# Kernel tuning notes

Measured on AMD Instinct MI355X. Metric: run time of the kernel, lower is better.

## Reference

```python
import jax, jax.numpy as jnp
import numpy as np
from jax import lax

I = 2048   # input_size
H = 2048   # hidden_size
T = 512    # window_size
L = 4      # num_layers


def setup_inputs() -> dict:
    key = jax.random.key(0)
    ks = jax.random.split(key, 8)
    s = 1.0 / np.sqrt(H)  # PyTorch RNN init scale
    x = jax.random.normal(ks[0], (I, T), dtype=jnp.float32)
    # input_size == hidden_size, so all layers' W_ih share shape (H, H)
    w_ih = jax.random.uniform(ks[1], (L, H, H), minval=-s, maxval=s, dtype=jnp.float32)
    w_hh = jax.random.uniform(ks[2], (L, H, H), minval=-s, maxval=s, dtype=jnp.float32)
    b_ih = jax.random.uniform(ks[3], (L, H), minval=-s, maxval=s, dtype=jnp.float32)
    b_hh = jax.random.uniform(ks[4], (L, H), minval=-s, maxval=s, dtype=jnp.float32)
    w_fc = jax.random.uniform(ks[5], (I, H), minval=-s, maxval=s, dtype=jnp.float32)
    b_fc = jax.random.uniform(ks[6], (I,), minval=-s, maxval=s, dtype=jnp.float32)
    return {"x": x, "w_ih": w_ih, "w_hh": w_hh, "b_ih": b_ih, "b_hh": b_hh,
            "w_fc": w_fc, "b_fc": b_fc}


def reference(x, w_ih, w_hh, b_ih, b_hh, w_fc, b_fc):
    # x: (input_size, window_size) -> seq: (T, I), matching x = x.T in torch
    seq = x.T
    n_layers = w_ih.shape[0]
    h_seq = seq
    for l in range(n_layers):
        # batched input projection for all timesteps: (T, H)
        pre = h_seq @ w_ih[l].T + b_ih[l]
        Whh = w_hh[l]
        bhh = b_hh[l]

        def step(h, p):
            h_new = jnp.tanh(p + h @ Whh.T + bhh)
            return h_new, h_new

        h0 = jnp.zeros((Whh.shape[0],), dtype=seq.dtype)
        _, h_seq = lax.scan(step, h0, pre)
        # nn.RNN's dropout=0.2 between layers is disabled in eval mode; omitted.
    # fc applied to last timestep only -> (input_size,)
    return h_seq[-1] @ w_fc.T + b_fc
```

## Files before the change

### kernel.cpp

```cpp
#include <hip/hip_runtime.h>
#include <math.h>


#define HH 2048
#define TT 512
#define NB 256
#define GRPB 128
#define NTH 512

typedef unsigned long long u64;
typedef unsigned int u32;

__device__ __forceinline__ u64 ld_a8(const float* p) {
  return __hip_atomic_load((const u64*)p, __ATOMIC_RELAXED,
                           __HIP_MEMORY_SCOPE_AGENT);
}
__device__ __forceinline__ void st_a4(float* p, float v) {
  __hip_atomic_store(p, v, __ATOMIC_RELAXED, __HIP_MEMORY_SCOPE_AGENT);
}
__device__ __forceinline__ bool fresh8(u64 v) {
  return ((u32)v != 0xFFFFFFFFu) & ((u32)(v >> 32) != 0xFFFFFFFFu);
}

__launch_bounds__(NTH, 2)
__global__ void rnn_pipe(const float* __restrict__ x,
                         const float* __restrict__ w_ih,
                         const float* __restrict__ w_hh,
                         const float* __restrict__ b_ih,
                         const float* __restrict__ b_hh,
                         const float* __restrict__ w_fc,
                         const float* __restrict__ b_fc,
                         float* __restrict__ out,
                         float* ws)
{
  const int blk  = blockIdx.x;
  const bool gA  = (blk < GRPB);
  const int gb   = gA ? blk : (blk - GRPB);
  const int tid  = threadIdx.x;
  const int wid  = tid >> 6;
  const int lane = tid & 63;
  const int band = wid >> 1;
  const int half = wid & 1;
  const int rowbase = gb * 16 + band * 4;

  __shared__ float hex_own[HH];
  __shared__ float hex_prev[HH];
  __shared__ float partial[8][4];

  const int sl = wid * 256 + lane * 4;

  for (int phase = 0; phase < 2; ++phase) {
    const int l = (phase == 0) ? (gA ? 0 : 1) : (gA ? 2 : 3);
    float* outB      = ws + (size_t)l * (TT + 1) * HH;
    const float* inB = (l == 0) ? (const float*)0
                                : ws + (size_t)(l - 1) * (TT + 1) * HH;

    float wih[4][16], whh[4][16];
#pragma unroll
    for (int r = 0; r < 4; ++r) {
      const float* pih = w_ih + ((size_t)l * HH + rowbase + r) * HH;
      const float* phh = w_hh + ((size_t)l * HH + rowbase + r) * HH;
#pragma unroll
      for (int k = 0; k < 8; ++k) {
        int c = half * 1024 + k * 128 + lane * 2;
        float2 a = *(const float2*)(pih + c);
        float2 b = *(const float2*)(phh + c);
        wih[r][2 * k] = a.x; wih[r][2 * k + 1] = a.y;
        whh[r][2 * k] = b.x; whh[r][2 * k + 1] = b.y;
      }
    }
    float fbias = 0.f;
    if (tid < 16)
      fbias = b_ih[l * HH + gb * 16 + tid] + b_hh[l * HH + gb * 16 + tid];

    for (int t = 0; t < TT; ++t) {
      const float* po = outB + (size_t)t * HH + sl;
      const float* pp = (l > 0) ? (inB + (size_t)(t + 1) * HH + sl)
                                : (const float*)0;
      u64 o0, o1, p0 = 0, p1 = 0;
      for (;;) {
        o0 = ld_a8(po);
        o1 = ld_a8(po + 2);
        if (l > 0) { p0 = ld_a8(pp); p1 = ld_a8(pp + 2); }
        bool ok = fresh8(o0) & fresh8(o1);
        if (l > 0) ok = ok & fresh8(p0) & fresh8(p1);
        if (__all(ok)) break;
        __builtin_amdgcn_s_sleep(2);
      }
      *(u64*)(hex_own + sl)     = o0;
      *(u64*)(hex_own + sl + 2) = o1;
      if (l > 0) {
        *(u64*)(hex_prev + sl)     = p0;
        *(u64*)(hex_prev + sl + 2) = p1;
      }
      __syncthreads();

      float hh[16], hi[16];
#pragma unroll
      for (int k = 0; k < 8; ++k) {
        int c = half * 1024 + k * 128 + lane * 2;
        float2 v = *(const float2*)(hex_own + c);
        hh[2 * k] = v.x; hh[2 * k + 1] = v.y;
      }
      if (l == 0) {
#pragma unroll
        for (int k = 0; k < 8; ++k) {
          int c = half * 1024 + k * 128 + lane * 2;
          hi[2 * k]     = x[(size_t)c * TT + t];
          hi[2 * k + 1] = x[(size_t)(c + 1) * TT + t];
        }
      } else {
#pragma unroll
        for (int k = 0; k < 8; ++k) {
          int c = half * 1024 + k * 128 + lane * 2;
          float2 v = *(const float2*)(hex_prev + c);
          hi[2 * k] = v.x; hi[2 * k + 1] = v.y;
        }
      }

      float a0 = 0.f, a1 = 0.f, a2 = 0.f, a3 = 0.f;
#pragma unroll
      for (int k = 0; k < 16; ++k) {
        a0 += whh[0][k] * hh[k]; a0 += wih[0][k] * hi[k];
        a1 += whh[1][k] * hh[k]; a1 += wih[1][k] * hi[k];
        a2 += whh[2][k] * hh[k]; a2 += wih[2][k] * hi[k];
        a3 += whh[3][k] * hh[k]; a3 += wih[3][k] * hi[k];
      }
#pragma unroll
      for (int m = 1; m < 64; m <<= 1) {
        a0 += __shfl_xor(a0, m, 64);
        a1 += __shfl_xor(a1, m, 64);
        a2 += __shfl_xor(a2, m, 64);
        a3 += __shfl_xor(a3, m, 64);
      }
      if (lane == 0) {
        partial[wid][0] = a0; partial[wid][1] = a1;
        partial[wid][2] = a2; partial[wid][3] = a3;
      }
      __syncthreads();
      if (tid < 16) {
        int bnd = tid >> 2, r = tid & 3;
        float s = partial[bnd * 2][r] + partial[bnd * 2 + 1][r] + fbias;
        st_a4(outB + (size_t)(t + 1) * HH + gb * 16 + tid, tanhf(s));
      }
    }
    __syncthreads();
  }

  if (gA) {
    const float* bufL3 = ws + (size_t)3 * (TT + 1) * HH;
    float wf[4][16];
#pragma unroll
    for (int r = 0; r < 4; ++r) {
      const float* pf = w_fc + (size_t)(rowbase + r) * HH;
#pragma unroll
      for (int k = 0; k < 8; ++k) {
        int c = half * 1024 + k * 128 + lane * 2;
        float2 a = *(const float2*)(pf + c);
        wf[r][2 * k] = a.x; wf[r][2 * k + 1] = a.y;
      }
    }
    const float* ph = bufL3 + (size_t)TT * HH + sl;
    u64 o0, o1;
    for (;;) {
      o0 = ld_a8(ph);
      o1 = ld_a8(ph + 2);
      if (__all(fresh8(o0) & fresh8(o1))) break;
      __builtin_amdgcn_s_sleep(2);
    }
    *(u64*)(hex_own + sl)     = o0;
    *(u64*)(hex_own + sl + 2) = o1;
    __syncthreads();

    float hv[16];
#pragma unroll
    for (int k = 0; k < 8; ++k) {
      int c = half * 1024 + k * 128 + lane * 2;
      float2 v = *(const float2*)(hex_own + c);
      hv[2 * k] = v.x; hv[2 * k + 1] = v.y;
    }
    float a0 = 0.f, a1 = 0.f, a2 = 0.f, a3 = 0.f;
#pragma unroll
    for (int k = 0; k < 16; ++k) {
      a0 += wf[0][k] * hv[k];
      a1 += wf[1][k] * hv[k];
      a2 += wf[2][k] * hv[k];
      a3 += wf[3][k] * hv[k];
    }
#pragma unroll
    for (int m = 1; m < 64; m <<= 1) {
      a0 += __shfl_xor(a0, m, 64);
      a1 += __shfl_xor(a1, m, 64);
      a2 += __shfl_xor(a2, m, 64);
      a3 += __shfl_xor(a3, m, 64);
    }
    if (lane == 0) {
      partial[wid][0] = a0; partial[wid][1] = a1;
      partial[wid][2] = a2; partial[wid][3] = a3;
    }
    __syncthreads();
    if (tid < 16) {
      int row = gb * 16 + tid;
      int bnd = tid >> 2, r = tid & 3;
      out[row] = partial[bnd * 2][r] + partial[bnd * 2 + 1][r] + b_fc[row];
    }
  }
}

extern "C" void kernel_launch(void* const* d_in, const int* in_sizes, int n_in,
                              void* d_out, int out_size, void* d_ws, size_t ws_size,
                              hipStream_t stream) {
  const float* x    = (const float*)d_in[0];
  const float* w_ih = (const float*)d_in[1];
  const float* w_hh = (const float*)d_in[2];
  const float* b_ih = (const float*)d_in[3];
  const float* b_hh = (const float*)d_in[4];
  const float* w_fc = (const float*)d_in[5];
  const float* b_fc = (const float*)d_in[6];
  float* out = (float*)d_out;
  float* ws  = (float*)d_ws;

  const size_t bufFloats = (size_t)(TT + 1) * HH;
  hipMemsetAsync(ws, 0xFF, 4 * bufFloats * sizeof(float), stream);
  for (int l = 0; l < 4; ++l)
    hipMemsetAsync(ws + l * bufFloats, 0, HH * sizeof(float), stream);

  rnn_pipe<<<NB, NTH, 0, stream>>>(x, w_ih, w_hh, b_ih, b_hh,
                                   w_fc, b_fc, out, ws);
}
```

Before: 6.316 ms.

## Run all four layers concurrently with 32-row blocks and bf16 input weights

Each layer now gets its own 64 blocks that run at the same time, so the layers form a wavefront pipeline instead of two sequential phases of two layers each. Every block owns 32 rows with a contiguous 4-column slice per thread. Hidden-state values stay in registers, which removes the LDS staging and one barrier. The input-weight rows are packed to bf16 so they fit in registers, and tanh uses an exp-based approximation; both lose some precision, and the transpose-style shuffle reduction adds shuffle work.

```diff
diff --git a/kernel.cpp b/kernel.cpp
--- a/kernel.cpp
+++ b/kernel.cpp
@@ -4,8 +4,9 @@
 
 #define HH 2048
 #define TT 512
-#define NB 256
-#define GRPB 128
+#define NBLK 256
+#define LBLK 64
+#define ROWS 32
 #define NTH 512
 
 typedef unsigned long long u64;
@@ -21,188 +22,173 @@
 __device__ __forceinline__ bool fresh8(u64 v) {
   return ((u32)v != 0xFFFFFFFFu) & ((u32)(v >> 32) != 0xFFFFFFFFu);
 }
+__device__ __forceinline__ u32 bf16rne(float f) {
+  u32 x = __float_as_uint(f);
+  return (x + 0x7fffu + ((x >> 16) & 1u)) >> 16;
+}
+__device__ __forceinline__ float bflo(u32 p) { return __uint_as_float(p << 16); }
+__device__ __forceinline__ float bfhi(u32 p) { return __uint_as_float(p & 0xffff0000u); }
+__device__ __forceinline__ float fast_tanh(float s) {
+  float e = __expf(2.f * s);
+  return 1.f - 2.f / (e + 1.f);
+}
 
 __launch_bounds__(NTH, 2)
-__global__ void rnn_pipe(const float* __restrict__ x,
-                         const float* __restrict__ w_ih,
-                         const float* __restrict__ w_hh,
-                         const float* __restrict__ b_ih,
-                         const float* __restrict__ b_hh,
-                         const float* __restrict__ w_fc,
-                         const float* __restrict__ b_fc,
-                         float* __restrict__ out,
-                         float* ws)
+__global__ void rnn_d4(const float* __restrict__ x,
+                       const float* __restrict__ w_ih,
+                       const float* __restrict__ w_hh,
+                       const float* __restrict__ b_ih,
+                       const float* __restrict__ b_hh,
+                       const float* __restrict__ w_fc,
+                       const float* __restrict__ b_fc,
+                       float* __restrict__ out,
+                       float* ws)
 {
   const int blk  = blockIdx.x;
-  const bool gA  = (blk < GRPB);
-  const int gb   = gA ? blk : (blk - GRPB);
+  const int l    = blk >> 6;
+  const int gb   = blk & (LBLK - 1);
   const int tid  = threadIdx.x;
   const int wid  = tid >> 6;
   const int lane = tid & 63;
-  const int band = wid >> 1;
-  const int half = wid & 1;
-  const int rowbase = gb * 16 + band * 4;
-
-  __shared__ float hex_own[HH];
-  __shared__ float hex_prev[HH];
-  __shared__ float partial[8][4];
-
-  const int sl = wid * 256 + lane * 4;
-
-  for (int phase = 0; phase < 2; ++phase) {
-    const int l = (phase == 0) ? (gA ? 0 : 1) : (gA ? 2 : 3);
-    float* outB      = ws + (size_t)l * (TT + 1) * HH;
-    const float* inB = (l == 0) ? (const float*)0
-                                : ws + (size_t)(l - 1) * (TT + 1) * HH;
-
-    float wih[4][16], whh[4][16];
-#pragma unroll
-    for (int r = 0; r < 4; ++r) {
-      const float* pih = w_ih + ((size_t)l * HH + rowbase + r) * HH;
-      const float* phh = w_hh + ((size_t)l * HH + rowbase + r) * HH;
-#pragma unroll
-      for (int k = 0; k < 8; ++k) {
-        int c = half * 1024 + k * 128 + lane * 2;
-        float2 a = *(const float2*)(pih + c);
-        float2 b = *(const float2*)(phh + c);
-        wih[r][2 * k] = a.x; wih[r][2 * k + 1] = a.y;
-        whh[r][2 * k] = b.x; whh[r][2 * k + 1] = b.y;
-      }
-    }
-    float fbias = 0.f;
-    if (tid < 16)
-      fbias = b_ih[l * HH + gb * 16 + tid] + b_hh[l * HH + gb * 16 + tid];
-
-    for (int t = 0; t < TT; ++t) {
-      const float* po = outB + (size_t)t * HH + sl;
-      const float* pp = (l > 0) ? (inB + (size_t)(t + 1) * HH + sl)
-                                : (const float*)0;
-      u64 o0, o1, p0 = 0, p1 = 0;
-      for (;;) {
-        o0 = ld_a8(po);
-        o1 = ld_a8(po + 2);
-        if (l > 0) { p0 = ld_a8(pp); p1 = ld_a8(pp + 2); }
-        bool ok = fresh8(o0) & fresh8(o1);
-        if (l > 0) ok = ok & fresh8(p0) & fresh8(p1);
-        if (__all(ok)) break;
-        __builtin_amdgcn_s_sleep(2);
-      }
-      *(u64*)(hex_own + sl)     = o0;
-      *(u64*)(hex_own + sl + 2) = o1;
-      if (l > 0) {
-        *(u64*)(hex_prev + sl)     = p0;
-        *(u64*)(hex_prev + sl + 2) = p1;
-      }
-      __syncthreads();
-
-      float hh[16], hi[16];
-#pragma unroll
-      for (int k = 0; k < 8; ++k) {
-        int c = half * 1024 + k * 128 + lane * 2;
-        float2 v = *(const float2*)(hex_own + c);
-        hh[2 * k] = v.x; hh[2 * k + 1] = v.y;
-      }
-      if (l == 0) {
-#pragma unroll
-        for (int k = 0; k < 8; ++k) {
-          int c = half * 1024 + k * 128 + lane * 2;
-          hi[2 * k]     = x[(size_t)c * TT + t];
-          hi[2 * k + 1] = x[(size_t)(c + 1) * TT + t];
-        }
-      } else {
-#pragma unroll
-        for (int k = 0; k < 8; ++k) {
-          int c = half * 1024 + k * 128 + lane * 2;
-          float2 v = *(const float2*)(hex_prev + c);
-          hi[2 * k] = v.x; hi[2 * k + 1] = v.y;
+  const int scol = wid * 256 + lane * 4;
+
+  float* outB      = ws + (size_t)l * (TT + 1) * HH;
+  const float* inB = ws + (size_t)(l - 1) * (TT + 1) * HH;
+
+  __shared__ float partial[2][8][32];
+
+  float whh[ROWS][4];
+  u32   wihp[ROWS][2];
+#pragma unroll
+  for (int r = 0; r < ROWS; ++r) {
+    const size_t rowoff = ((size_t)l * HH + gb * ROWS + r) * HH + scol;
+    const float4 vh = *(const float4*)(w_hh + rowoff);
+    whh[r][0] = vh.x; whh[r][1] = vh.y; whh[r][2] = vh.z; whh[r][3] = vh.w;
+    const float4 vi = *(const float4*)(w_ih + rowoff);
+    wihp[r][0] = bf16rne(vi.x) | (bf16rne(vi.y) << 16);
+    wihp[r][1] = bf16rne(vi.z) | (bf16rne(vi.w) << 16);
+  }
+  float fbias = 0.f;
+  if (wid == 0 && lane < 32)
+    fbias = b_ih[l * HH + gb * ROWS + lane] + b_hh[l * HH + gb * ROWS + lane];
+
+  const int rrow = ((lane & 1) << 4) | ((lane & 2) << 2) | (lane & 4) |
+                   ((lane & 8) >> 2) | ((lane & 16) >> 4);
+
+  const float* po = outB + scol;
+  const float* pp = inB + HH + scol;
+  float* ps = outB + HH + gb * ROWS + lane;
+  const float* xb = x + (size_t)scol * TT;
+
+  for (int t = 0; t < TT; ++t) {
+    float xg0 = 0.f, xg1 = 0.f, xg2 = 0.f, xg3 = 0.f;
+    if (l == 0) {
+      xg0 = xb[0 * TT + t]; xg1 = xb[1 * TT + t];
+      xg2 = xb[2 * TT + t]; xg3 = xb[3 * TT + t];
+    }
+
+    u64 o0, o1, p0 = 0, p1 = 0;
+    for (;;) {
+      o0 = ld_a8(po);
+      o1 = ld_a8(po + 2);
+      if (l > 0) { p0 = ld_a8(pp); p1 = ld_a8(pp + 2); }
+      bool ok = fresh8(o0) & fresh8(o1);
+      if (l > 0) ok = ok & fresh8(p0) & fresh8(p1);
+      if (__all(ok)) break;
+      __builtin_amdgcn_s_sleep(1);
+    }
+    float hh0 = __uint_as_float((u32)o0), hh1 = __uint_as_float((u32)(o0 >> 32));
+    float hh2 = __uint_as_float((u32)o1), hh3 = __uint_as_float((u32)(o1 >> 32));
+    float hi0, hi1, hi2, hi3;
+    if (l == 0) { hi0 = xg0; hi1 = xg1; hi2 = xg2; hi3 = xg3; }
+    else {
+      hi0 = __uint_as_float((u32)p0); hi1 = __uint_as_float((u32)(p0 >> 32));
+      hi2 = __uint_as_float((u32)p1); hi3 = __uint_as_float((u32)(p1 >> 32));
+    }
+
+    float acc[ROWS];
+#pragma unroll
+    for (int r = 0; r < ROWS; ++r) {
+      float a = whh[r][0] * hh0 + whh[r][1] * hh1 +
+                whh[r][2] * hh2 + whh[r][3] * hh3;
+      a += bflo(wihp[r][0]) * hi0 + bfhi(wihp[r][0]) * hi1;
+      a += bflo(wihp[r][1]) * hi2 + bfhi(wihp[r][1]) * hi3;
+      acc[r] = a;
+    }
+
+#pragma unroll
+    for (int i = 0; i < 32; ++i) acc[i] += __shfl_xor(acc[i], 32, 64);
+#pragma unroll
+    for (int lv = 0; lv < 5; ++lv) {
+      const int m = 1 << lv;
+      const int n = 16 >> lv;
+      const bool up = (lane & m) != 0;
+#pragma unroll
+      for (int i = 0; i < 16; ++i) {
+        if (i < n) {
+          float mine   = up ? acc[i + n] : acc[i];
+          float theirs = __shfl_xor(up ? acc[i] : acc[i + n], m, 64);
+          acc[i] = mine + theirs;
         }
       }
-
-      float a0 = 0.f, a1 = 0.f, a2 = 0.f, a3 = 0.f;
-#pragma unroll
-      for (int k = 0; k < 16; ++k) {
-        a0 += whh[0][k] * hh[k]; a0 += wih[0][k] * hi[k];
-        a1 += whh[1][k] * hh[k]; a1 += wih[1][k] * hi[k];
-        a2 += whh[2][k] * hh[k]; a2 += wih[2][k] * hi[k];
-        a3 += whh[3][k] * hh[k]; a3 += wih[3][k] * hi[k];
-      }
-#pragma unroll
-      for (int m = 1; m < 64; m <<= 1) {
-        a0 += __shfl_xor(a0, m, 64);
-        a1 += __shfl_xor(a1, m, 64);
-        a2 += __shfl_xor(a2, m, 64);
-        a3 += __shfl_xor(a3, m, 64);
-      }
-      if (lane == 0) {
-        partial[wid][0] = a0; partial[wid][1] = a1;
-        partial[wid][2] = a2; partial[wid][3] = a3;
-      }
-      __syncthreads();
-      if (tid < 16) {
-        int bnd = tid >> 2, r = tid & 3;
-        float s = partial[bnd * 2][r] + partial[bnd * 2 + 1][r] + fbias;
-        st_a4(outB + (size_t)(t + 1) * HH + gb * 16 + tid, tanhf(s));
-      }
-    }
+    }
+    if (lane < 32) partial[t & 1][wid][rrow] = acc[0];
     __syncthreads();
+
+    if (wid == 0 && lane < 32) {
+      float s = fbias;
+#pragma unroll
+      for (int w = 0; w < 8; ++w) s += partial[t & 1][w][lane];
+      st_a4(ps, fast_tanh(s));
+    }
+    po += HH; pp += HH; ps += HH;
   }
 
-  if (gA) {
-    const float* bufL3 = ws + (size_t)3 * (TT + 1) * HH;
-    float wf[4][16];
-#pragma unroll
-    for (int r = 0; r < 4; ++r) {
-      const float* pf = w_fc + (size_t)(rowbase + r) * HH;
-#pragma unroll
-      for (int k = 0; k < 8; ++k) {
-        int c = half * 1024 + k * 128 + lane * 2;
-        float2 a = *(const float2*)(pf + c);
-        wf[r][2 * k] = a.x; wf[r][2 * k + 1] = a.y;
-      }
-    }
-    const float* ph = bufL3 + (size_t)TT * HH + sl;
+  if (l == 3) {
+    float wf[ROWS][4];
+#pragma unroll
+    for (int r = 0; r < ROWS; ++r) {
+      const float4 v = *(const float4*)(w_fc + (size_t)(gb * ROWS + r) * HH + scol);
+      wf[r][0] = v.x; wf[r][1] = v.y; wf[r][2] = v.z; wf[r][3] = v.w;
+    }
+    const float* ph = outB + (size_t)TT * HH + scol;
     u64 o0, o1;
     for (;;) {
       o0 = ld_a8(ph);
       o1 = ld_a8(ph + 2);
       if (__all(fresh8(o0) & fresh8(o1))) break;
-      __builtin_amdgcn_s_sleep(2);
-    }
-    *(u64*)(hex_own + sl)     = o0;
-    *(u64*)(hex_own + sl + 2) = o1;
+      __builtin_amdgcn_s_sleep(1);
+    }
+    float h0 = __uint_as_float((u32)o0), h1 = __uint_as_float((u32)(o0 >> 32));
+    float h2 = __uint_as_float((u32)o1), h3 = __uint_as_float((u32)(o1 >> 32));
+
+    float acc[ROWS];
+#pragma unroll
+    for (int r = 0; r < ROWS; ++r)
+      acc[r] = wf[r][0] * h0 + wf[r][1] * h1 + wf[r][2] * h2 + wf[r][3] * h3;
+#pragma unroll
+    for (int i = 0; i < 32; ++i) acc[i] += __shfl_xor(acc[i], 32, 64);
+#pragma unroll
+    for (int lv = 0; lv < 5; ++lv) {
+      const int m = 1 << lv;
+      const int n = 16 >> lv;
+      const bool up = (lane & m) != 0;
+#pragma unroll
+      for (int i = 0; i < 16; ++i) {
+        if (i < n) {
+          float mine   = up ? acc[i + n] : acc[i];
+          float theirs = __shfl_xor(up ? acc[i] : acc[i + n], m, 64);
+          acc[i] = mine + theirs;
+        }
+      }
+    }
+    if (lane < 32) partial[0][wid][rrow] = acc[0];
     __syncthreads();
-
-    float hv[16];
-#pragma unroll
-    for (int k = 0; k < 8; ++k) {
-      int c = half * 1024 + k * 128 + lane * 2;
-      float2 v = *(const float2*)(hex_own + c);
-      hv[2 * k] = v.x; hv[2 * k + 1] = v.y;
-    }
-    float a0 = 0.f, a1 = 0.f, a2 = 0.f, a3 = 0.f;
-#pragma unroll
-    for (int k = 0; k < 16; ++k) {
-      a0 += wf[0][k] * hv[k];
-      a1 += wf[1][k] * hv[k];
-      a2 += wf[2][k] * hv[k];
-      a3 += wf[3][k] * hv[k];
-    }
-#pragma unroll
-    for (int m = 1; m < 64; m <<= 1) {
-      a0 += __shfl_xor(a0, m, 64);
-      a1 += __shfl_xor(a1, m, 64);
-      a2 += __shfl_xor(a2, m, 64);
-      a3 += __shfl_xor(a3, m, 64);
-    }
-    if (lane == 0) {
-      partial[wid][0] = a0; partial[wid][1] = a1;
-      partial[wid][2] = a2; partial[wid][3] = a3;
-    }
-    __syncthreads();
-    if (tid < 16) {
-      int row = gb * 16 + tid;
-      int bnd = tid >> 2, r = tid & 3;
-      out[row] = partial[bnd * 2][r] + partial[bnd * 2 + 1][r] + b_fc[row];
+    if (wid == 0 && lane < 32) {
+      float s = b_fc[gb * ROWS + lane];
+#pragma unroll
+      for (int w = 0; w < 8; ++w) s += partial[0][w][lane];
+      out[gb * ROWS + lane] = s;
     }
   }
 }
@@ -225,6 +211,6 @@
   for (int l = 0; l < 4; ++l)
     hipMemsetAsync(ws + l * bufFloats, 0, HH * sizeof(float), stream);
 
-  rnn_pipe<<<NB, NTH, 0, stream>>>(x, w_ih, w_hh, b_ih, b_hh,
+  rnn_d4<<<NBLK, NTH, 0, stream>>>(x, w_ih, w_hh, b_ih, b_hh,
                                    w_fc, b_fc, out, ws);
 }
```

Measured after the change: 19.35 ms. +206.4%, slower.
